# Kernel tuning notes

Hardware: AMD Instinct MI355X
Metric: run time of the kernel (lower is better)

The kernel has to match this reference:

```python
import jax, jax.numpy as jnp
import numpy as np
from jax import lax

EPS = 1e-5
K = 3            # FreqFilter kernel size
G = 8            # groups = out_ch // channel_per_group = 64 // 8


def conv2d(x, w, pad):
    return lax.conv_general_dilated(
        x, w, window_strides=(1, 1), padding=[(pad, pad), (pad, pad)],
        dimension_numbers=("NCHW", "OIHW", "NCHW"))


def leaky(x):
    return jnp.where(x >= 0, x, 0.01 * x)


def freq_filter(y, wf, gamma, beta):
    # y: (n, c, h, w) with c = 64
    n, c, h, w = y.shape
    yp = jnp.pad(y, ((0, 0), (0, 0), (1, 1), (1, 1)), mode="reflect")
    sig = conv2d(yp, wf, pad=0)                       # (n, G*K*K, h, w)
    # BatchNorm2d in training mode: batch statistics over (N,H,W)
    mu = sig.mean(axis=(0, 2, 3), keepdims=True)
    var = sig.var(axis=(0, 2, 3), keepdims=True)
    sig = (sig - mu) * lax.rsqrt(var + EPS)
    sig = sig * gamma[None, :, None, None] + beta[None, :, None, None]
    sig = jax.nn.softmax(sig, axis=1)                 # softmax over all G*K*K channels
    sig = sig.reshape(n, G, K * K, h, w)              # channel = g*(K*K) + k
    # kernel = identity (delta at center tap) - sigma
    center = K * K // 2
    delta = jnp.zeros((K * K,), sig.dtype).at[center].set(1.0)
    kernel = delta[None, None, :, None, None] - sig   # (n, G, 9, h, w)
    # im2col patches of the reflect-padded input, unfold ordering (row-major taps)
    patches = jnp.stack(
        [yp[:, :, i:i + h, j:j + w] for i in range(K) for j in range(K)],
        axis=2)                                        # (n, c, 9, h, w)
    patches = patches.reshape(n, G, c // G, K * K, h, w)
    out = jnp.einsum("ngckhw,ngkhw->ngchw", patches, kernel)
    return out.reshape(n, c, h, w)


def hin(x):
    # InstanceNorm2d (affine=False) on first half of channels
    half = x.shape[1] // 2
    a = x[:, :half]
    mu = a.mean(axis=(2, 3), keepdims=True)
    var = a.var(axis=(2, 3), keepdims=True)
    a = (a - mu) * lax.rsqrt(var + EPS)
    return jnp.concatenate([a, x[:, half:]], axis=1)


def setup_inputs() -> dict:
    key = jax.random.key(0)
    ks = jax.random.split(key, 8)
    n, cin, cout, h, w = 4, 64, 64, 256, 256
    return {
        "x": jax.random.normal(ks[0], (n, cin, h, w), jnp.float32),
        "w1": jax.random.normal(ks[1], (cout, cin, 3, 3), jnp.float32) * 0.05,
        "b1": jax.random.normal(ks[2], (cout,), jnp.float32) * 0.01,
        "wf": jax.random.normal(ks[3], (G * K * K, cout, 3, 3), jnp.float32) * 0.06,
        "bn_gamma": jnp.ones((G * K * K,), jnp.float32),
        "bn_beta": jnp.zeros((G * K * K,), jnp.float32),
        "w2": jax.random.normal(ks[4], (cout, cout, 3, 3), jnp.float32) * 0.05,
        "b2": jax.random.normal(ks[5], (cout,), jnp.float32) * 0.01,
        "wr": jax.random.normal(ks[6], (cout, cin, 1, 1), jnp.float32) * 0.1,
        "br": jax.random.normal(ks[7], (cout,), jnp.float32) * 0.01,
    }


def reference(x, w1, b1, wf, bn_gamma, bn_beta, w2, b2, wr, br):
    y = conv2d(x, w1, pad=1) + b1[None, :, None, None]
    y = freq_filter(y, wf, bn_gamma, bn_beta)
    y = leaky(hin(y))
    y = leaky(conv2d(y, w2, pad=1) + b2[None, :, None, None])
    res = conv2d(x, wr, pad=0) + br[None, :, None, None]
    return res + y
```

## Files before the change

### kernel.cpp

```cpp
#include <hip/hip_runtime.h>

typedef unsigned short u16;
typedef __attribute__((ext_vector_type(8))) short bf16x8;
typedef __attribute__((ext_vector_type(4))) float f32x4;
typedef __attribute__((address_space(3))) void lds_void;
typedef __attribute__((address_space(1))) const void gbl_void;

#define NN 4
#define HH 256
#define WW 256
#define PD 258
#define CIN 64
#define EPSV 1e-5f

__device__ __forceinline__ float b2f(u16 x){ union{unsigned u; float f;} q; q.u = ((unsigned)x)<<16; return q.f; }
__device__ __forceinline__ u16 f2b(float f){ union{float f; unsigned u;} q; q.f = f; unsigned r = q.u + 0x7FFF + ((q.u>>16)&1u); return (u16)(r>>16); }
__device__ __forceinline__ float leakyf(float x){ return x >= 0.f ? x : 0.01f*x; }

__global__ void prep_kernel(const float* __restrict__ w1, const float* __restrict__ wf,
                            const float* __restrict__ w2, const float* __restrict__ wr,
                            u16* __restrict__ wB1, u16* __restrict__ wBf,
                            u16* __restrict__ wB2, u16* __restrict__ wBr){
  int idx = blockIdx.x*256 + threadIdx.x;
  if (idx < 36864){
    int e = idx & 7, lane = (idx >> 3) & 63, q = idx >> 9;
    int f = q & 3, ksq = q >> 2, ks = ksq & 1, tap = ksq >> 1;
    int cout = f*16 + (lane & 15);
    int cin  = ks*32 + (lane >> 4)*8 + e;
    wB1[idx] = f2b(w1[(cout*64 + cin)*9 + tap]);
    wB2[idx] = f2b(w2[(cout*64 + cin)*9 + tap]);
  }
  if (idx < 46080){
    int e = idx & 7, lane = (idx >> 3) & 63, q = idx >> 9;
    int f = q % 5, ksq = q / 5, ks = ksq & 1, tap = ksq >> 1;
    int cout = f*16 + (lane & 15);
    int cin  = ks*32 + (lane >> 4)*8 + e;
    float v = (cout < 72) ? wf[(cout*64 + cin)*9 + tap] : 0.f;
    wBf[idx] = f2b(v);
  }
  if (idx < 4096){
    int e = idx & 7, lane = (idx >> 3) & 63, q = idx >> 9;
    int f = q & 3, ks = q >> 2;
    int cout = f*16 + (lane & 15);
    int cin  = ks*32 + (lane >> 4)*8 + e;
    wBr[idx] = f2b(wr[cout*64 + cin]);
  }
}

__global__ __launch_bounds__(256) void padx_kernel(const float* __restrict__ x, u16* __restrict__ xpad){
  int n = blockIdx.x >> 8, h = blockIdx.x & 255, t = threadIdx.x;
  u16* dstrow = xpad + ((size_t)(n*PD + h + 1)*PD)*CIN;
  const uint4 z = {0,0,0,0};
  #pragma unroll
  for (int c8 = 0; c8 < 8; ++c8){
    u16 buf[8];
    #pragma unroll
    for (int j = 0; j < 8; ++j)
      buf[j] = f2b(x[((size_t)(n*64 + c8*8 + j))*65536 + h*256 + t]);
    *(uint4*)(dstrow + (size_t)(t+1)*CIN + c8*8) = *(uint4*)buf;
  }
  if (t == 0)   { for (int c8 = 0; c8 < 8; ++c8) *(uint4*)(dstrow + 0*CIN   + c8*8) = z; }
  if (t == 255) { for (int c8 = 0; c8 < 8; ++c8) *(uint4*)(dstrow + 257*CIN + c8*8) = z; }
  if (h == 0 || h == 255){
    u16* brow = xpad + ((size_t)(n*PD + (h == 0 ? 0 : 257))*PD)*CIN;
    for (int p = t; p < PD; p += 256)
      for (int c8 = 0; c8 < 8; ++c8) *(uint4*)(brow + (size_t)p*CIN + c8*8) = z;
  }
}

__global__ void reflect_kernel(u16* __restrict__ y1pad){
  int idx = blockIdx.x*256 + threadIdx.x;
  if (idx >= 4*1028*8) return;
  int n = idx/(1028*8), rem = idx%(1028*8), p = rem >> 3, cc = rem & 7;
  int pr, pc;
  if      (p < 258)  { pr = 0;   pc = p; }
  else if (p < 516)  { pr = 257; pc = p - 258; }
  else if (p < 772)  { pr = 1 + (p - 516); pc = 0; }
  else               { pr = 1 + (p - 772); pc = 257; }
  int sr = (pr == 0) ? 2 : ((pr == 257) ? 255 : pr);
  int sc = (pc == 0) ? 2 : ((pc == 257) ? 255 : pc);
  uint4 v = *(const uint4*)(y1pad + ((size_t)(n*PD + sr)*PD + sc)*CIN + cc*8);
  *(uint4*)(y1pad + ((size_t)(n*PD + pr)*PD + pc)*CIN + cc*8) = v;
}

template<int NF, int MODE>
__global__ __launch_bounds__(256, 4) void conv_mfma(
    const u16* __restrict__ Ain, const u16* __restrict__ wB, const float* __restrict__ bias,
    u16* __restrict__ outB, float* __restrict__ outF,
    const u16* __restrict__ xpad, const u16* __restrict__ wBr,
    const float* __restrict__ br,
    float* __restrict__ bnsum, float* __restrict__ bnsumsq){

  constexpr int NC  = NF*16;
  constexpr int NCP = NC + 8;
  __shared__ __align__(16) char smem[2112*16];

  int t = threadIdx.x, lane = t & 63, wv = t >> 6;
  int bid = blockIdx.x;
  int sb = (bid & 7)*256 + (bid >> 3);
  int n = sb >> 9, rem = sb & 511, rowb = rem >> 2, colb = rem & 3;
  int h0 = rowb*2, w0 = colb*64;
  int l15 = lane & 15, l4 = lane >> 4;
  int r = wv >> 1, ch = wv & 1;

  {
    const u16* base = Ain + ((size_t)(n*PD + h0)*PD + w0)*CIN;
    #pragma unroll
    for (int rnd = 0; rnd < 9; ++rnd){
      if (rnd < 8 || wv == 0){
        int c = rnd*256 + wv*64 + lane;
        int row = c / 528, rem2 = c - row*528;
        int px = rem2 >> 3, sub = rem2 & 7;
        int subs = sub ^ (px & 7);
        const u16* src = base + (size_t)row*PD*CIN + (size_t)(px*8 + subs)*8;
        __builtin_amdgcn_global_load_lds((gbl_void*)src,
                                         (lds_void*)(smem + (rnd*256 + wv*64)*16), 16, 0, 0);
      }
    }
  }
  __syncthreads();

  f32x4 acc[2][NF];
  #pragma unroll
  for (int mf = 0; mf < 2; ++mf)
    #pragma unroll
    for (int f = 0; f < NF; ++f) acc[mf][f] = (f32x4){0.f,0.f,0.f,0.f};

  #pragma unroll
  for (int tap = 0; tap < 9; ++tap){
    const int dh = tap/3, dw = tap%3;
    #pragma unroll
    for (int ks = 0; ks < 2; ++ks){
      bf16x8 wfr[NF];
      #pragma unroll
      for (int f = 0; f < NF; ++f)
        wfr[f] = *(const bf16x8*)(wB + ((size_t)(((tap*2 + ks)*NF + f)*64 + lane))*8);
      #pragma unroll
      for (int mf = 0; mf < 2; ++mf){
        int wcol = ch*32 + mf*16 + l15 + dw;
        int wrow = r + dh;
        int j  = ks*4 + l4;
        bf16x8 afr = *(const bf16x8*)(smem + ((((wrow*66 + wcol) << 3) + (j ^ (wcol & 7))) << 4));
        #pragma unroll
        for (int f = 0; f < NF; ++f)
          acc[mf][f] = __builtin_amdgcn_mfma_f32_16x16x32_bf16(afr, wfr[f], acc[mf][f], 0, 0, 0);
      }
    }
  }

  if (MODE < 2){
    __syncthreads();
    u16* Bx = (u16*)smem;
    float* bnpart = (float*)(smem + 24576);
    if (MODE == 1){
      #pragma unroll
      for (int f = 0; f < NF; ++f){
        float s = 0.f, q = 0.f;
        #pragma unroll
        for (int mf = 0; mf < 2; ++mf)
          #pragma unroll
          for (int reg = 0; reg < 4; ++reg){ float v = acc[mf][f][reg]; s += v; q += v*v; }
        s += __shfl_xor(s, 16); q += __shfl_xor(q, 16);
        s += __shfl_xor(s, 32); q += __shfl_xor(q, 32);
        if (l4 == 0){
          bnpart[((wv*NF + f)*16 + l15)*2 + 0] = s;
          bnpart[((wv*NF + f)*16 + l15)*2 + 1] = q;
        }
      }
    }
    #pragma unroll
    for (int mf = 0; mf < 2; ++mf)
      #pragma unroll
      for (int f = 0; f < NF; ++f){
        int cout = f*16 + l15;
        float bv = (MODE == 0) ? bias[cout] : 0.f;
        #pragma unroll
        for (int reg = 0; reg < 4; ++reg){
          int px = r*64 + ch*32 + mf*16 + l4*4 + reg;
          Bx[px*NCP + cout] = f2b(acc[mf][f][reg] + bv);
        }
      }
    __syncthreads();
    const int nch = NC/8;
    for (int idx = t; idx < 128*nch; idx += 256){
      int px = idx/nch, c8 = idx - px*nch;
      int rr = px >> 6, cc = px & 63;
      uint4 v = *(const uint4*)(Bx + px*NCP + c8*8);
      if (MODE == 0)
        *(uint4*)(outB + ((size_t)(n*PD + h0 + 1 + rr)*PD + (w0 + 1 + cc))*CIN + c8*8) = v;
      else
        *(uint4*)(outB + ((size_t)(n*65536 + (h0 + rr)*256 + w0 + cc))*80 + c8*8) = v;
    }
    if (MODE == 1 && t < 160){
      int c = t >> 1, which = t & 1;
      if (c < 72){
        int fi = c >> 4, li = c & 15;
        float v = bnpart[((0*NF + fi)*16 + li)*2 + which] + bnpart[((1*NF + fi)*16 + li)*2 + which]
                + bnpart[((2*NF + fi)*16 + li)*2 + which] + bnpart[((3*NF + fi)*16 + li)*2 + which];
        atomicAdd(which ? &bnsumsq[c] : &bnsum[c], v);
      }
    }
  } else {
    const u16* Xn = xpad + ((size_t)(n*PD + h0 + 1 + r)*PD + w0 + 1)*CIN;
    #pragma unroll
    for (int mf = 0; mf < 2; ++mf){
      int pxc = ch*32 + mf*16 + l15;
      bf16x8 xf0 = *(const bf16x8*)(Xn + (size_t)pxc*CIN + l4*8);
      bf16x8 xf1 = *(const bf16x8*)(Xn + (size_t)pxc*CIN + 32 + l4*8);
      #pragma unroll
      for (int f = 0; f < NF; ++f){
        int cout = f*16 + l15;
        bf16x8 b0 = *(const bf16x8*)(wBr + ((size_t)((0*NF + f)*64 + lane))*8);
        bf16x8 b1 = *(const bf16x8*)(wBr + ((size_t)((1*NF + f)*64 + lane))*8);
        f32x4 tmp = (f32x4){0.f,0.f,0.f,0.f};
        tmp = __builtin_amdgcn_mfma_f32_16x16x32_bf16(xf0, b0, tmp, 0, 0, 0);
        tmp = __builtin_amdgcn_mfma_f32_16x16x32_bf16(xf1, b1, tmp, 0, 0, 0);
        float bv = bias[cout], bb = br[cout];
        float4 o;
        o.x = leakyf(acc[mf][f][0] + bv) + tmp[0] + bb;
        o.y = leakyf(acc[mf][f][1] + bv) + tmp[1] + bb;
        o.z = leakyf(acc[mf][f][2] + bv) + tmp[2] + bb;
        o.w = leakyf(acc[mf][f][3] + bv) + tmp[3] + bb;
        int px = ch*32 + mf*16 + l4*4;
        *(float4*)(outF + ((size_t)(n*64 + cout))*65536 + (h0 + r)*256 + w0 + px) = o;
      }
    }
  }
}

__global__ void bnfinal_kernel(const float* __restrict__ bnsum, const float* __restrict__ bnsumsq,
                               const float* __restrict__ gamma, const float* __restrict__ beta,
                               float* __restrict__ bnscale, float* __restrict__ bnshift){
  int c = threadIdx.x;
  if (c < 72){
    const float M = 262144.f;
    float mu  = bnsum[c] / M;
    float var = bnsumsq[c] / M - mu*mu;
    float sc  = gamma[c] * rsqrtf(var + EPSV);
    bnscale[c] = sc;
    bnshift[c] = beta[c] - mu*sc;
  }
}

__global__ __launch_bounds__(256, 4) void filter_kernel(const u16* __restrict__ sig,
                                                        const u16* __restrict__ y1pad,
                                                        const float* __restrict__ bnscale,
                                                        const float* __restrict__ bnshift,
                                                        u16* __restrict__ y2pad,
                                                        float* __restrict__ hinsum,
                                                        float* __restrict__ hinsumsq){
  __shared__ __align__(16) char smem[2112*16];
  __shared__ float sc[72], sh[72];

  int t = threadIdx.x, lane = t & 63, wv = t >> 6;
  if (t < 72){ sc[t] = bnscale[t]; sh[t] = bnshift[t]; }
  int bid = blockIdx.x;
  int sb = (bid & 7)*256 + (bid >> 3);
  int n = sb >> 9, rem = sb & 511, rowb = rem >> 2, colb = rem & 3;
  int h0 = rowb*2, w0 = colb*64;
  int p = t & 127, r = p >> 6, c = p & 63, half = t >> 7;

  {
    const u16* base = y1pad + ((size_t)(n*PD + h0)*PD + w0)*CIN;
    #pragma unroll
    for (int rnd = 0; rnd < 9; ++rnd){
      if (rnd < 8 || wv == 0){
        int cch = rnd*256 + wv*64 + lane;
        int row = cch / 528, rem2 = cch - row*528;
        int px = rem2 >> 3, sub = rem2 & 7;
        int subs = sub ^ (px & 7);
        const u16* src = base + (size_t)row*PD*CIN + (size_t)(px*8 + subs)*8;
        __builtin_amdgcn_global_load_lds((gbl_void*)src,
                                         (lds_void*)(smem + (rnd*256 + wv*64)*16), 16, 0, 0);
      }
    }
  }

  float sv[72];
  const u16* sp = sig + ((size_t)(n*65536 + (h0 + r)*256 + w0 + c))*80;
  #pragma unroll
  for (int i = 0; i < 9; ++i){
    uint4 v = *(const uint4*)(sp + i*8);
    const u16* e = (const u16*)&v;
    #pragma unroll
    for (int j = 0; j < 8; ++j) sv[i*8+j] = b2f(e[j]);
  }
  __syncthreads();
  float mx = -1e30f;
  #pragma unroll
  for (int cc = 0; cc < 72; ++cc){ sv[cc] = sv[cc]*sc[cc] + sh[cc]; mx = fmaxf(mx, sv[cc]); }
  float sum = 0.f;
  #pragma unroll
  for (int cc = 0; cc < 72; ++cc){ sv[cc] = __expf(sv[cc] - mx); sum += sv[cc]; }
  float inv = -1.f/sum;
  float kv[36];
  if (half == 0){
    #pragma unroll
    for (int j = 0; j < 36; ++j) kv[j] = sv[j]*inv;
  } else {
    #pragma unroll
    for (int j = 0; j < 36; ++j) kv[j] = sv[36 + j]*inv;
  }
  #pragma unroll
  for (int c8 = 0; c8 < 4; ++c8) kv[c8*9 + 4] += 1.f;

  float o[32];
  #pragma unroll
  for (int cc = 0; cc < 32; ++cc) o[cc] = 0.f;
  #pragma unroll
  for (int i = 0; i < 3; ++i){
    #pragma unroll
    for (int j = 0; j < 3; ++j){
      int wcol = c + j, wrow = r + i;
      #pragma unroll
      for (int c8 = 0; c8 < 4; ++c8){
        int chunk = half*4 + c8;
        uint4 v = *(const uint4*)(smem + ((((wrow*66 + wcol) << 3) + (chunk ^ (wcol & 7))) << 4));
        const u16* e = (const u16*)&v;
        float k = kv[c8*9 + i*3 + j];
        #pragma unroll
        for (int jj = 0; jj < 8; ++jj) o[c8*8 + jj] = fmaf(k, b2f(e[jj]), o[c8*8 + jj]);
      }
    }
  }
  __syncthreads();

  u16* obuf = (u16*)smem;
  float* ps = (float*)(smem + 20480);
  #pragma unroll
  for (int c8 = 0; c8 < 4; ++c8){
    u16 ob[8];
    #pragma unroll
    for (int jj = 0; jj < 8; ++jj) ob[jj] = f2b(o[c8*8 + jj]);
    *(uint4*)(obuf + p*66 + (half*4 + c8)*8) = *(uint4*)ob;
  }
  __syncthreads();

  {
    int cch = t & 31, seg = t >> 5;
    float s = 0.f, q = 0.f;
    #pragma unroll
    for (int rr = 0; rr < 16; ++rr){
      float v = b2f(obuf[(seg*16 + rr)*66 + cch]);
      s += v; q += v*v;
    }
    ps[(seg*32 + cch)*2 + 0] = s; ps[(seg*32 + cch)*2 + 1] = q;
  }
  for (int idx = t; idx < 1024; idx += 256){
    int pp = idx >> 3, j = idx & 7;
    int rr = pp >> 6, cc = pp & 63;
    uint4 v = *(const uint4*)(obuf + pp*66 + j*8);
    *(uint4*)(y2pad + ((size_t)(n*PD + h0 + 1 + rr)*PD + (w0 + 1 + cc))*CIN + j*8) = v;
  }
  __syncthreads();
  if (t < 64){
    int cc = t >> 1, which = t & 1;
    float v = 0.f;
    #pragma unroll
    for (int seg = 0; seg < 8; ++seg) v += ps[(seg*32 + cc)*2 + which];
    atomicAdd(which ? &hinsumsq[n*32 + cc] : &hinsum[n*32 + cc], v);
  }
}

__global__ void hinfinal_kernel(const float* __restrict__ hinsum, const float* __restrict__ hinsumsq,
                                float* __restrict__ hmu, float* __restrict__ hrs){
  int i = threadIdx.x;
  if (i < 128){
    const float M = 65536.f;
    float mu  = hinsum[i] / M;
    float var = hinsumsq[i] / M - mu*mu;
    hmu[i] = mu;
    hrs[i] = rsqrtf(var + EPSV);
  }
}

__global__ __launch_bounds__(256) void hinapply_kernel(u16* __restrict__ y2pad,
                                                       const float* __restrict__ hmu,
                                                       const float* __restrict__ hrs){
  int n = blockIdx.x / PD, pr = blockIdx.x % PD, t = threadIdx.x;
  u16* row = y2pad + (size_t)(n*PD + pr)*PD*CIN;
  bool ringrow = (pr == 0) || (pr == PD-1);
  for (int idx = t; idx < PD*8; idx += 256){
    int px = idx >> 3, cc = idx & 7;
    uint4* p = (uint4*)(row + (size_t)px*CIN + cc*8);
    if (ringrow || px == 0 || px == PD-1){
      uint4 z = {0,0,0,0}; *p = z; continue;
    }
    uint4 v = *p;
    u16* e = (u16*)&v;
    if (cc < 4){
      int cb = n*32 + cc*8;
      #pragma unroll
      for (int j = 0; j < 8; ++j){
        float f = (b2f(e[j]) - hmu[cb+j]) * hrs[cb+j];
        e[j] = f2b(leakyf(f));
      }
    } else {
      #pragma unroll
      for (int j = 0; j < 8; ++j) e[j] = f2b(leakyf(b2f(e[j])));
    }
    *p = v;
  }
}

extern "C" void kernel_launch(void* const* d_in, const int* in_sizes, int n_in,
                              void* d_out, int out_size, void* d_ws, size_t ws_size,
                              hipStream_t stream){
  const float* x     = (const float*)d_in[0];
  const float* w1    = (const float*)d_in[1];
  const float* b1    = (const float*)d_in[2];
  const float* wf    = (const float*)d_in[3];
  const float* gamma = (const float*)d_in[4];
  const float* beta  = (const float*)d_in[5];
  const float* w2    = (const float*)d_in[6];
  const float* b2    = (const float*)d_in[7];
  const float* wr    = (const float*)d_in[8];
  const float* br    = (const float*)d_in[9];

  char* ws = (char*)d_ws;
  const size_t PADB = (size_t)NN*PD*PD*CIN*2;
  u16* xpad  = (u16*)(ws);
  u16* y1pad = (u16*)(ws + PADB);
  u16* y2pad = (u16*)(ws + 2*PADB);
  float* stats = (float*)(ws + 3*PADB);
  float* bnsum   = stats;        float* bnsumsq = stats + 80;
  float* bnscale = stats + 160;  float* bnshift = stats + 240;
  float* hinsum  = stats + 320;  float* hinsumsq= stats + 448;
  float* hmu     = stats + 576;  float* hrs     = stats + 704;
  u16* wB1 = (u16*)(ws + 3*PADB + 4096);
  u16* wBf = wB1 + 36864;
  u16* wB2 = wBf + 46080;
  u16* wBr = wB2 + 36864;

  u16* sig = (u16*)d_out;
  float* out = (float*)d_out;

  hipMemsetAsync(stats, 0, 4096, stream);
  prep_kernel<<<180, 256, 0, stream>>>(w1, wf, w2, wr, wB1, wBf, wB2, wBr);
  padx_kernel<<<NN*HH, 256, 0, stream>>>(x, xpad);
  conv_mfma<4,0><<<2048, 256, 0, stream>>>(xpad, wB1, b1, y1pad, nullptr, nullptr, nullptr, nullptr, nullptr, nullptr);
  reflect_kernel<<<(4*1028*8 + 255)/256, 256, 0, stream>>>(y1pad);
  conv_mfma<5,1><<<2048, 256, 0, stream>>>(y1pad, wBf, nullptr, sig, nullptr, nullptr, nullptr, nullptr, bnsum, bnsumsq);
  bnfinal_kernel<<<1, 80, 0, stream>>>(bnsum, bnsumsq, gamma, beta, bnscale, bnshift);
  filter_kernel<<<2048, 256, 0, stream>>>(sig, y1pad, bnscale, bnshift, y2pad, hinsum, hinsumsq);
  hinfinal_kernel<<<1, 128, 0, stream>>>(hinsum, hinsumsq, hmu, hrs);
  hinapply_kernel<<<NN*PD, 256, 0, stream>>>(y2pad, hmu, hrs);
  conv_mfma<4,2><<<2048, 256, 0, stream>>>(y2pad, wB2, b2, nullptr, out, xpad, wBr, br, nullptr, nullptr);
}
```

Before: 228.5 us.

## Switch conv kernels to 32x32x16 MFMA with channel-group wave split

Rewrites the three conv kernels to use 32x32x16 bf16 MFMA instead of 16x16x32. Each wave now owns a 32-output-channel group and one pixel row, and the weight prep is repacked to match. The filter-sigma conv runs 3 channel groups (96 padded outputs, 384 threads) instead of 5x16. The larger MFMA tile gives more reuse per A/B fragment and fewer LDS reads per FLOP. The cost is extra padded work on the 72-channel conv and higher register pressure.

```diff
diff --git a/kernel.cpp b/kernel.cpp
--- a/kernel.cpp
+++ b/kernel.cpp
@@ -2,7 +2,7 @@
 
 typedef unsigned short u16;
 typedef __attribute__((ext_vector_type(8))) short bf16x8;
-typedef __attribute__((ext_vector_type(4))) float f32x4;
+typedef __attribute__((ext_vector_type(16))) float f32x16;
 typedef __attribute__((address_space(3))) void lds_void;
 typedef __attribute__((address_space(1))) const void gbl_void;
 
@@ -23,26 +23,29 @@
                             u16* __restrict__ wB2, u16* __restrict__ wBr){
   int idx = blockIdx.x*256 + threadIdx.x;
   if (idx < 36864){
-    int e = idx & 7, lane = (idx >> 3) & 63, q = idx >> 9;
-    int f = q & 3, ksq = q >> 2, ks = ksq & 1, tap = ksq >> 1;
-    int cout = f*16 + (lane & 15);
-    int cin  = ks*32 + (lane >> 4)*8 + e;
-    wB1[idx] = f2b(w1[(cout*64 + cin)*9 + tap]);
-    wB2[idx] = f2b(w2[(cout*64 + cin)*9 + tap]);
-  }
-  if (idx < 46080){
-    int e = idx & 7, lane = (idx >> 3) & 63, q = idx >> 9;
-    int f = q % 5, ksq = q / 5, ks = ksq & 1, tap = ksq >> 1;
-    int cout = f*16 + (lane & 15);
-    int cin  = ks*32 + (lane >> 4)*8 + e;
+    int e = idx & 7, lane = (idx >> 3) & 63, rest = idx >> 9;
+    int tap = rest % 9, rest2 = rest / 9;
+    int cg = rest2 & 1, kq = rest2 >> 1;
+    int cout = cg*32 + (lane & 31);
+    int cin  = kq*16 + (lane >> 5)*8 + e;
+    int src = (cout*64 + cin)*9 + tap;
+    wB1[idx] = f2b(w1[src]);
+    wB2[idx] = f2b(w2[src]);
+  }
+  if (idx < 55296){
+    int e = idx & 7, lane = (idx >> 3) & 63, rest = idx >> 9;
+    int tap = rest % 9, rest2 = rest / 9;
+    int cg = rest2 % 3, kq = rest2 / 3;
+    int cout = cg*32 + (lane & 31);
+    int cin  = kq*16 + (lane >> 5)*8 + e;
     float v = (cout < 72) ? wf[(cout*64 + cin)*9 + tap] : 0.f;
     wBf[idx] = f2b(v);
   }
   if (idx < 4096){
-    int e = idx & 7, lane = (idx >> 3) & 63, q = idx >> 9;
-    int f = q & 3, ks = q >> 2;
-    int cout = f*16 + (lane & 15);
-    int cin  = ks*32 + (lane >> 4)*8 + e;
+    int e = idx & 7, lane = (idx >> 3) & 63, rest = idx >> 9;
+    int cg = rest & 1, kq = rest >> 1;
+    int cout = cg*32 + (lane & 31);
+    int cin  = kq*16 + (lane >> 5)*8 + e;
     wBr[idx] = f2b(wr[cout*64 + cin]);
   }
 }
@@ -83,106 +86,100 @@
   *(uint4*)(y1pad + ((size_t)(n*PD + pr)*PD + pc)*CIN + cc*8) = v;
 }
 
-template<int NF, int MODE>
-__global__ __launch_bounds__(256, 4) void conv_mfma(
+template<int NCG, int MODE>
+__global__ __launch_bounds__(NCG*128, 4) void conv_mfma(
     const u16* __restrict__ Ain, const u16* __restrict__ wB, const float* __restrict__ bias,
     u16* __restrict__ outB, float* __restrict__ outF,
     const u16* __restrict__ xpad, const u16* __restrict__ wBr,
     const float* __restrict__ br,
     float* __restrict__ bnsum, float* __restrict__ bnsumsq){
 
-  constexpr int NC  = NF*16;
+  constexpr int NC  = (MODE == 1) ? 80 : 64;
   constexpr int NCP = NC + 8;
+  constexpr int TPB = NCG*128;
+  constexpr int NW  = NCG*2;
+  constexpr int RND = (2112 + TPB - 1)/TPB;
   __shared__ __align__(16) char smem[2112*16];
 
   int t = threadIdx.x, lane = t & 63, wv = t >> 6;
+  int l31 = lane & 31, l1 = lane >> 5;
+  int cg = wv % NCG, ph = wv / NCG;
   int bid = blockIdx.x;
   int sb = (bid & 7)*256 + (bid >> 3);
   int n = sb >> 9, rem = sb & 511, rowb = rem >> 2, colb = rem & 3;
   int h0 = rowb*2, w0 = colb*64;
-  int l15 = lane & 15, l4 = lane >> 4;
-  int r = wv >> 1, ch = wv & 1;
 
   {
     const u16* base = Ain + ((size_t)(n*PD + h0)*PD + w0)*CIN;
     #pragma unroll
-    for (int rnd = 0; rnd < 9; ++rnd){
-      if (rnd < 8 || wv == 0){
-        int c = rnd*256 + wv*64 + lane;
+    for (int rnd = 0; rnd < RND; ++rnd){
+      int c = rnd*TPB + wv*64 + lane;
+      if (c < 2112){
         int row = c / 528, rem2 = c - row*528;
         int px = rem2 >> 3, sub = rem2 & 7;
         int subs = sub ^ (px & 7);
         const u16* src = base + (size_t)row*PD*CIN + (size_t)(px*8 + subs)*8;
         __builtin_amdgcn_global_load_lds((gbl_void*)src,
-                                         (lds_void*)(smem + (rnd*256 + wv*64)*16), 16, 0, 0);
+                                         (lds_void*)(smem + (size_t)c*16), 16, 0, 0);
       }
     }
   }
   __syncthreads();
 
-  f32x4 acc[2][NF];
-  #pragma unroll
-  for (int mf = 0; mf < 2; ++mf)
-    #pragma unroll
-    for (int f = 0; f < NF; ++f) acc[mf][f] = (f32x4){0.f,0.f,0.f,0.f};
-
-  #pragma unroll
-  for (int tap = 0; tap < 9; ++tap){
-    const int dh = tap/3, dw = tap%3;
-    #pragma unroll
-    for (int ks = 0; ks < 2; ++ks){
-      bf16x8 wfr[NF];
-      #pragma unroll
-      for (int f = 0; f < NF; ++f)
-        wfr[f] = *(const bf16x8*)(wB + ((size_t)(((tap*2 + ks)*NF + f)*64 + lane))*8);
-      #pragma unroll
-      for (int mf = 0; mf < 2; ++mf){
-        int wcol = ch*32 + mf*16 + l15 + dw;
-        int wrow = r + dh;
-        int j  = ks*4 + l4;
-        bf16x8 afr = *(const bf16x8*)(smem + ((((wrow*66 + wcol) << 3) + (j ^ (wcol & 7))) << 4));
-        #pragma unroll
-        for (int f = 0; f < NF; ++f)
-          acc[mf][f] = __builtin_amdgcn_mfma_f32_16x16x32_bf16(afr, wfr[f], acc[mf][f], 0, 0, 0);
-      }
-    }
-  }
+  f32x16 acc[2];
+  #pragma unroll
+  for (int pg = 0; pg < 2; ++pg)
+    #pragma unroll
+    for (int i = 0; i < 16; ++i) acc[pg][i] = 0.f;
+
+  #pragma unroll
+  for (int kq = 0; kq < 4; ++kq){
+    bf16x8 wfr[9];
+    #pragma unroll
+    for (int tap = 0; tap < 9; ++tap)
+      wfr[tap] = *(const bf16x8*)(wB + ((size_t)((kq*NCG + cg)*9 + tap)*64 + lane)*8);
+    #pragma unroll
+    for (int pg = 0; pg < 2; ++pg){
+      #pragma unroll
+      for (int tap = 0; tap < 9; ++tap){
+        int wrow = ph + tap/3;
+        int wcol = pg*32 + l31 + tap%3;
+        int chunk = (kq*2 + l1) ^ (wcol & 7);
+        bf16x8 afr = *(const bf16x8*)(smem + ((((wrow*66 + wcol) << 3) + chunk) << 4));
+        acc[pg] = __builtin_amdgcn_mfma_f32_32x32x16_bf16(afr, wfr[tap], acc[pg], 0, 0, 0);
+      }
+    }
+  }
+
+  int cout = cg*32 + l31;
 
   if (MODE < 2){
     __syncthreads();
     u16* Bx = (u16*)smem;
     float* bnpart = (float*)(smem + 24576);
     if (MODE == 1){
-      #pragma unroll
-      for (int f = 0; f < NF; ++f){
-        float s = 0.f, q = 0.f;
+      float s = 0.f, q = 0.f;
+      #pragma unroll
+      for (int pg = 0; pg < 2; ++pg)
         #pragma unroll
-        for (int mf = 0; mf < 2; ++mf)
-          #pragma unroll
-          for (int reg = 0; reg < 4; ++reg){ float v = acc[mf][f][reg]; s += v; q += v*v; }
-        s += __shfl_xor(s, 16); q += __shfl_xor(q, 16);
-        s += __shfl_xor(s, 32); q += __shfl_xor(q, 32);
-        if (l4 == 0){
-          bnpart[((wv*NF + f)*16 + l15)*2 + 0] = s;
-          bnpart[((wv*NF + f)*16 + l15)*2 + 1] = q;
-        }
-      }
-    }
-    #pragma unroll
-    for (int mf = 0; mf < 2; ++mf)
-      #pragma unroll
-      for (int f = 0; f < NF; ++f){
-        int cout = f*16 + l15;
-        float bv = (MODE == 0) ? bias[cout] : 0.f;
-        #pragma unroll
-        for (int reg = 0; reg < 4; ++reg){
-          int px = r*64 + ch*32 + mf*16 + l4*4 + reg;
-          Bx[px*NCP + cout] = f2b(acc[mf][f][reg] + bv);
-        }
-      }
+        for (int reg = 0; reg < 16; ++reg){ float v = acc[pg][reg]; s += v; q += v*v; }
+      s += __shfl_xor(s, 32); q += __shfl_xor(q, 32);
+      if (l1 == 0){ bnpart[(wv*32 + l31)*2 + 0] = s; bnpart[(wv*32 + l31)*2 + 1] = q; }
+    }
+    #pragma unroll
+    for (int pg = 0; pg < 2; ++pg){
+      float bv = (MODE == 0) ? bias[cout] : 0.f;
+      #pragma unroll
+      for (int reg = 0; reg < 16; ++reg){
+        int rowD = (reg & 3) + 8*(reg >> 2) + 4*l1;
+        int p = ph*64 + pg*32 + rowD;
+        if (MODE == 0 || cout < 80)
+          Bx[p*NCP + cout] = f2b(acc[pg][reg] + bv);
+      }
+    }
     __syncthreads();
-    const int nch = NC/8;
-    for (int idx = t; idx < 128*nch; idx += 256){
+    constexpr int nch = NC/8;
+    for (int idx = t; idx < 128*nch; idx += TPB){
       int px = idx/nch, c8 = idx - px*nch;
       int rr = px >> 6, cc = px & 63;
       uint4 v = *(const uint4*)(Bx + px*NCP + c8*8);
@@ -191,38 +188,43 @@
       else
         *(uint4*)(outB + ((size_t)(n*65536 + (h0 + rr)*256 + w0 + cc))*80 + c8*8) = v;
     }
-    if (MODE == 1 && t < 160){
+    if (MODE == 1 && t < 192){
       int c = t >> 1, which = t & 1;
       if (c < 72){
-        int fi = c >> 4, li = c & 15;
-        float v = bnpart[((0*NF + fi)*16 + li)*2 + which] + bnpart[((1*NF + fi)*16 + li)*2 + which]
-                + bnpart[((2*NF + fi)*16 + li)*2 + which] + bnpart[((3*NF + fi)*16 + li)*2 + which];
+        int cgf = c >> 5, ci = c & 31;
+        float v = bnpart[((cgf*32) + ci)*2 + which] + bnpart[(((NCG + cgf)*32) + ci)*2 + which];
         atomicAdd(which ? &bnsumsq[c] : &bnsum[c], v);
       }
     }
   } else {
-    const u16* Xn = xpad + ((size_t)(n*PD + h0 + 1 + r)*PD + w0 + 1)*CIN;
-    #pragma unroll
-    for (int mf = 0; mf < 2; ++mf){
-      int pxc = ch*32 + mf*16 + l15;
-      bf16x8 xf0 = *(const bf16x8*)(Xn + (size_t)pxc*CIN + l4*8);
-      bf16x8 xf1 = *(const bf16x8*)(Xn + (size_t)pxc*CIN + 32 + l4*8);
-      #pragma unroll
-      for (int f = 0; f < NF; ++f){
-        int cout = f*16 + l15;
-        bf16x8 b0 = *(const bf16x8*)(wBr + ((size_t)((0*NF + f)*64 + lane))*8);
-        bf16x8 b1 = *(const bf16x8*)(wBr + ((size_t)((1*NF + f)*64 + lane))*8);
-        f32x4 tmp = (f32x4){0.f,0.f,0.f,0.f};
-        tmp = __builtin_amdgcn_mfma_f32_16x16x32_bf16(xf0, b0, tmp, 0, 0, 0);
-        tmp = __builtin_amdgcn_mfma_f32_16x16x32_bf16(xf1, b1, tmp, 0, 0, 0);
-        float bv = bias[cout], bb = br[cout];
+    f32x16 racc[2];
+    #pragma unroll
+    for (int pg = 0; pg < 2; ++pg)
+      #pragma unroll
+      for (int i = 0; i < 16; ++i) racc[pg][i] = 0.f;
+    const u16* Xrow = xpad + ((size_t)(n*PD + h0 + 1 + ph)*PD + (w0 + 1))*CIN;
+    #pragma unroll
+    for (int kq = 0; kq < 4; ++kq){
+      bf16x8 wr8 = *(const bf16x8*)(wBr + ((size_t)((kq*2 + cg)*64 + lane))*8);
+      #pragma unroll
+      for (int pg = 0; pg < 2; ++pg){
+        bf16x8 xfr = *(const bf16x8*)(Xrow + (size_t)(pg*32 + l31)*CIN + kq*16 + l1*8);
+        racc[pg] = __builtin_amdgcn_mfma_f32_32x32x16_bf16(xfr, wr8, racc[pg], 0, 0, 0);
+      }
+    }
+    float bv = bias[cout], bb = br[cout];
+    float* orow = outF + ((size_t)(n*64 + cout))*65536 + (h0 + ph)*256 + w0;
+    #pragma unroll
+    for (int pg = 0; pg < 2; ++pg){
+      #pragma unroll
+      for (int q = 0; q < 4; ++q){
         float4 o;
-        o.x = leakyf(acc[mf][f][0] + bv) + tmp[0] + bb;
-        o.y = leakyf(acc[mf][f][1] + bv) + tmp[1] + bb;
-        o.z = leakyf(acc[mf][f][2] + bv) + tmp[2] + bb;
-        o.w = leakyf(acc[mf][f][3] + bv) + tmp[3] + bb;
-        int px = ch*32 + mf*16 + l4*4;
-        *(float4*)(outF + ((size_t)(n*64 + cout))*65536 + (h0 + r)*256 + w0 + px) = o;
+        o.x = leakyf(acc[pg][q*4+0] + bv) + racc[pg][q*4+0] + bb;
+        o.y = leakyf(acc[pg][q*4+1] + bv) + racc[pg][q*4+1] + bb;
+        o.z = leakyf(acc[pg][q*4+2] + bv) + racc[pg][q*4+2] + bb;
+        o.w = leakyf(acc[pg][q*4+3] + bv) + racc[pg][q*4+3] + bb;
+        int px = pg*32 + 8*q + 4*l1;
+        *(float4*)(orow + px) = o;
       }
     }
   }
@@ -429,21 +431,21 @@
   float* hmu     = stats + 576;  float* hrs     = stats + 704;
   u16* wB1 = (u16*)(ws + 3*PADB + 4096);
   u16* wBf = wB1 + 36864;
-  u16* wB2 = wBf + 46080;
+  u16* wB2 = wBf + 55296;
   u16* wBr = wB2 + 36864;
 
   u16* sig = (u16*)d_out;
   float* out = (float*)d_out;
 
   hipMemsetAsync(stats, 0, 4096, stream);
-  prep_kernel<<<180, 256, 0, stream>>>(w1, wf, w2, wr, wB1, wBf, wB2, wBr);
+  prep_kernel<<<256, 256, 0, stream>>>(w1, wf, w2, wr, wB1, wBf, wB2, wBr);
   padx_kernel<<<NN*HH, 256, 0, stream>>>(x, xpad);
-  conv_mfma<4,0><<<2048, 256, 0, stream>>>(xpad, wB1, b1, y1pad, nullptr, nullptr, nullptr, nullptr, nullptr, nullptr);
+  conv_mfma<2,0><<<2048, 256, 0, stream>>>(xpad, wB1, b1, y1pad, nullptr, nullptr, nullptr, nullptr, nullptr, nullptr);
   reflect_kernel<<<(4*1028*8 + 255)/256, 256, 0, stream>>>(y1pad);
-  conv_mfma<5,1><<<2048, 256, 0, stream>>>(y1pad, wBf, nullptr, sig, nullptr, nullptr, nullptr, nullptr, bnsum, bnsumsq);
+  conv_mfma<3,1><<<2048, 384, 0, stream>>>(y1pad, wBf, nullptr, sig, nullptr, nullptr, nullptr, nullptr, bnsum, bnsumsq);
   bnfinal_kernel<<<1, 80, 0, stream>>>(bnsum, bnsumsq, gamma, beta, bnscale, bnshift);
   filter_kernel<<<2048, 256, 0, stream>>>(sig, y1pad, bnscale, bnshift, y2pad, hinsum, hinsumsq);
   hinfinal_kernel<<<1, 128, 0, stream>>>(hinsum, hinsumsq, hmu, hrs);
   hinapply_kernel<<<NN*PD, 256, 0, stream>>>(y2pad, hmu, hrs);
-  conv_mfma<4,2><<<2048, 256, 0, stream>>>(y2pad, wB2, b2, nullptr, out, xpad, wBr, br, nullptr, nullptr);
-}
+  conv_mfma<2,2><<<2048, 256, 0, stream>>>(y2pad, wB2, b2, nullptr, out, xpad, wBr, br, nullptr, nullptr);
+}
```

Result: no change. 227.0 us (-0.6%).
